# Performance work log

Measured on AMD Instinct MI355X. Metric: run time of the kernel, lower is better.

The kernel has to match this reference:

```python
import jax, jax.numpy as jnp
import numpy as np

D_MODEL = 1024
NUM_HEADS = 16
HEAD_DIM = D_MODEL // NUM_HEADS


def setup_inputs() -> dict:
    key = jax.random.key(0)
    ks = jax.random.split(key, 9)
    B, S = 2, 2048
    s = 1.0 / np.sqrt(D_MODEL)
    inp = {
        "x": jax.random.normal(ks[0], (B, S, D_MODEL), dtype=jnp.float32),
        "Wq": jax.random.normal(ks[1], (D_MODEL, D_MODEL), dtype=jnp.float32) * s,
        "bq": jnp.zeros((D_MODEL,), dtype=jnp.float32),
        "Wk": jax.random.normal(ks[2], (D_MODEL, D_MODEL), dtype=jnp.float32) * s,
        "bk": jnp.zeros((D_MODEL,), dtype=jnp.float32),
        "Wv": jax.random.normal(ks[3], (D_MODEL, D_MODEL), dtype=jnp.float32) * s,
        "bv": jnp.zeros((D_MODEL,), dtype=jnp.float32),
        "Wo": jax.random.normal(ks[4], (D_MODEL, D_MODEL), dtype=jnp.float32) * s,
        "bo": jnpp if False else jnp.zeros((D_MODEL,), dtype=jnp.float32),
    }
    return inp


def reference(x, Wq, bq, Wk, bk, Wv, bv, Wo, bo):
    B, S, D = x.shape
    H, hd = NUM_HEADS, HEAD_DIM
    # QKV projections (Linear: x @ W^T + b), split into heads -> [B,H,S,hd]
    q = (x @ Wq.T + bq).reshape(B, S, H, hd).transpose(0, 2, 1, 3)
    k = (x @ Wk.T + bk).reshape(B, S, H, hd).transpose(0, 2, 1, 3)
    v = (x @ Wv.T + bv).reshape(B, S, H, hd).transpose(0, 2, 1, 3)
    # scores [B,H,S,S]
    scores = jnp.einsum('bhqd,bhkd->bhqk', q, k) / jnp.sqrt(jnp.float32(hd))
    p = jax.nn.softmax(scores, axis=-1)
    out = jnp.einsum('bhqk,bhkd->bhqd', p, v)  # [B,H,S,hd]
    out = out.transpose(0, 2, 1, 3).reshape(B, S, D)
    return out @ Wo.T + bo
```

## Files before the change

### kernel.cpp

```cpp
#include <hip/hip_runtime.h>
#include <hip/hip_bf16.h>
#include <math.h>

typedef __bf16 bf16;
typedef unsigned short u16;
typedef __bf16 bf16x8 __attribute__((ext_vector_type(8)));
typedef __bf16 bf16x4 __attribute__((ext_vector_type(4)));
typedef short  s16x4  __attribute__((ext_vector_type(4)));
typedef float  f32x4  __attribute__((ext_vector_type(4)));

#define D_MODEL 1024
#define NHEAD   16
#define HD      64
#define BATCH   2
#define SEQ     2048
#define MTOT    (BATCH*SEQ)

#define EXPSCALE 0.18033688011116016f

__device__ __forceinline__ void async16(const void* g, void* l) {
    __builtin_amdgcn_global_load_lds(
        (__attribute__((address_space(1))) unsigned int*)g,
        (__attribute__((address_space(3))) unsigned int*)l,
        16, 0, 0);
}

__device__ __forceinline__ f32x4 mfma16(s16x4 a, s16x4 b, f32x4 c) {
    return __builtin_amdgcn_mfma_f32_16x16x16bf16_1k(a, b, c, 0, 0, 0);
}

__global__ __launch_bounds__(256) void cast_kernel(
    const float* __restrict__ x,
    const float* __restrict__ wq, const float* __restrict__ wk,
    const float* __restrict__ wv, const float* __restrict__ wo,
    bf16* __restrict__ xb, bf16* __restrict__ wqb, bf16* __restrict__ wkb,
    bf16* __restrict__ wvb, bf16* __restrict__ wob)
{
    const int z = blockIdx.y;
    const float* src;
    bf16* dst;
    int n;
    if (z == 0)      { src = x;  dst = xb;  n = MTOT * D_MODEL; }
    else if (z == 1) { src = wq; dst = wqb; n = D_MODEL * D_MODEL; }
    else if (z == 2) { src = wk; dst = wkb; n = D_MODEL * D_MODEL; }
    else if (z == 3) { src = wv; dst = wvb; n = D_MODEL * D_MODEL; }
    else             { src = wo; dst = wob; n = D_MODEL * D_MODEL; }

    int i = (blockIdx.x * 256 + threadIdx.x) * 8;
    if (i >= n) return;
    float4 a = *(const float4*)(src + i);
    float4 b = *(const float4*)(src + i + 4);
    bf16x8 o;
    o[0] = (bf16)a.x; o[1] = (bf16)a.y; o[2] = (bf16)a.z; o[3] = (bf16)a.w;
    o[4] = (bf16)b.x; o[5] = (bf16)b.y; o[6] = (bf16)b.z; o[7] = (bf16)b.w;
    *(bf16x8*)(dst + i) = o;
}

__device__ __forceinline__ void gemm_core(const bf16* __restrict__ A,
                                          const bf16* __restrict__ W,
                                          int m0, int n0,
                                          f32x4 acc[4][4],
                                          u16* lA, u16* lB)
{
    const int tid  = threadIdx.x;
    const int lane = tid & 63;
    const int wave = tid >> 6;
    const int wr   = wave >> 1;
    const int wc   = wave & 1;
    const int fr   = lane & 15;
    const int quad = lane >> 4;
    const int sa   = (quad ^ (fr & 3)) * 8;

    #pragma unroll
    for (int mi = 0; mi < 4; ++mi)
        #pragma unroll
        for (int ni = 0; ni < 4; ++ni)
            #pragma unroll
            for (int e = 0; e < 4; ++e)
                acc[mi][ni][e] = 0.0f;

    const int row0 = tid >> 2;
    const int row1 = row0 + 64;
    const int ca   = ((tid & 3) ^ (row0 & 3)) * 8;
    const bf16* gA0 = A + (size_t)(m0 + row0) * 1024 + ca;
    const bf16* gA1 = A + (size_t)(m0 + row1) * 1024 + ca;
    const bf16* gB0 = W + (size_t)(n0 + row0) * 1024 + ca;
    const bf16* gB1 = W + (size_t)(n0 + row1) * 1024 + ca;
    u16* sA0 = lA + (size_t)tid * 8;
    u16* sA1 = lA + (size_t)(tid + 256) * 8;
    u16* sB0 = lB + (size_t)tid * 8;
    u16* sB1 = lB + (size_t)(tid + 256) * 8;

    for (int kt = 0; kt < 1024 / 32; ++kt) {
        __syncthreads();
        async16(gA0 + kt * 32, sA0);
        async16(gA1 + kt * 32, sA1);
        async16(gB0 + kt * 32, sB0);
        async16(gB1 + kt * 32, sB1);
        __syncthreads();

        bf16x8 af[4], bfm[4];
        #pragma unroll
        for (int mi = 0; mi < 4; ++mi)
            af[mi] = *(const bf16x8*)(lA + (wr * 64 + mi * 16 + fr) * 32 + sa);
        #pragma unroll
        for (int ni = 0; ni < 4; ++ni)
            bfm[ni] = *(const bf16x8*)(lB + (wc * 64 + ni * 16 + fr) * 32 + sa);

        #pragma unroll
        for (int mi = 0; mi < 4; ++mi)
            #pragma unroll
            for (int ni = 0; ni < 4; ++ni)
                acc[mi][ni] = __builtin_amdgcn_mfma_f32_16x16x32_bf16(
                    af[mi], bfm[ni], acc[mi][ni], 0, 0, 0);
    }
}

__global__ __launch_bounds__(256) void qkv_kernel(
    const bf16* __restrict__ x,
    const bf16* __restrict__ Wq, const bf16* __restrict__ Wk, const bf16* __restrict__ Wv,
    const float* __restrict__ bq, const float* __restrict__ bk, const float* __restrict__ bv,
    bf16* __restrict__ Q, bf16* __restrict__ K, bf16* __restrict__ Vt)
{
    __shared__ __align__(16) u16 lA[128 * 32];
    __shared__ __align__(16) u16 lB[128 * 32];

    const int z  = blockIdx.z;
    const float* bias = (z == 0) ? bq : (z == 1) ? bk : bv;

    int m0, n0;
    const bf16 *mA, *mB;
    if (z == 2) {
        mA = Wv; mB = x;
        m0 = blockIdx.y * 128;
        n0 = blockIdx.x * 128;
    } else {
        mA = x;  mB = (z == 0) ? Wq : Wk;
        m0 = blockIdx.x * 128;
        n0 = blockIdx.y * 128;
    }

    f32x4 acc[4][4];
    gemm_core(mA, mB, m0, n0, acc, lA, lB);

    const int lane = threadIdx.x & 63;
    const int wave = threadIdx.x >> 6;
    const int wr = wave >> 1, wc = wave & 1;
    const int col = lane & 15, quad = lane >> 4;

    if (z == 2) {
        #pragma unroll
        for (int mi = 0; mi < 4; ++mi) {
            #pragma unroll
            for (int ni = 0; ni < 4; ++ni) {
                #pragma unroll
                for (int r = 0; r < 4; ++r) {
                    int f = m0 + wr * 64 + mi * 16 + quad * 4 + r;
                    int t = n0 + wc * 64 + ni * 16 + col;
                    float v = acc[mi][ni][r] + bias[f];
                    int b = t >> 11, s = t & 2047;
                    int h = f >> 6,  d = f & 63;
                    Vt[((size_t)(b * NHEAD + h) * HD + d) * SEQ + s] = (bf16)v;
                }
            }
        }
    } else {
        const float qs = (z == 0) ? EXPSCALE : 1.0f;
        bf16* o = (z == 0) ? Q : K;
        #pragma unroll
        for (int mi = 0; mi < 4; ++mi) {
            #pragma unroll
            for (int ni = 0; ni < 4; ++ni) {
                #pragma unroll
                for (int r = 0; r < 4; ++r) {
                    int m = m0 + wr * 64 + mi * 16 + quad * 4 + r;
                    int n = n0 + wc * 64 + ni * 16 + col;
                    float v = (acc[mi][ni][r] + bias[n]) * qs;
                    int b = m >> 11, s = m & 2047;
                    int h = n >> 6,  d = n & 63;
                    o[((size_t)(b * NHEAD + h) * SEQ + s) * HD + d] = (bf16)v;
                }
            }
        }
    }
}

__global__ __launch_bounds__(256, 4) void attn_kernel(
    const bf16* __restrict__ Q, const bf16* __restrict__ K,
    const bf16* __restrict__ Vt, bf16* __restrict__ O)
{
    __shared__ __align__(16) u16 lK[64 * 64];
    __shared__ __align__(16) u16 lV[64 * 64];

    const int tid  = threadIdx.x;
    const int lane = tid & 63;
    const int wave = tid >> 6;
    const int col  = lane & 15;
    const int quad = lane >> 4;
    const int bh   = blockIdx.y;
    const int q0   = blockIdx.x * 64;

    const bf16* Qh = Q  + (size_t)bh * SEQ * HD;
    const bf16* Kh = K  + (size_t)bh * SEQ * HD;
    const bf16* Vh = Vt + (size_t)bh * HD * SEQ;

    bf16x8 qf[2];
    #pragma unroll
    for (int ks = 0; ks < 2; ++ks)
        qf[ks] = *(const bf16x8*)(
            Qh + (size_t)(q0 + wave * 16 + col) * HD + ks * 32 + quad * 8);

    f32x4 acc_o[4];
    #pragma unroll
    for (int nd = 0; nd < 4; ++nd)
        #pragma unroll
        for (int e = 0; e < 4; ++e) acc_o[nd][e] = 0.0f;
    float rs = 0.0f;
    const f32x4 zero4 = {0.0f, 0.0f, 0.0f, 0.0f};

    const int r0 = tid >> 3;
    const int r1 = r0 + 32;
    const int g0 = (((tid & 7) ^ (r0 & 7))) * 8;
    const int g1 = (((tid & 7) ^ (r1 & 7))) * 8;
    const bf16* gK0 = Kh + (size_t)r0 * HD + g0;
    const bf16* gK1 = Kh + (size_t)r1 * HD + g1;
    const bf16* gV0 = Vh + (size_t)r0 * SEQ + g0;
    const bf16* gV1 = Vh + (size_t)r1 * SEQ + g1;
    u16* sK0 = lK + (size_t)tid * 8;
    u16* sK1 = lK + (size_t)(tid + 256) * 8;
    u16* sV0 = lV + (size_t)tid * 8;
    u16* sV1 = lV + (size_t)(tid + 256) * 8;

    for (int jt = 0; jt < SEQ / 64; ++jt) {
        __syncthreads();
        async16(gK0 + (size_t)jt * 64 * HD, sK0);
        async16(gK1 + (size_t)jt * 64 * HD, sK1);
        async16(gV0 + jt * 64, sV0);
        async16(gV1 + jt * 64, sV1);
        __syncthreads();

        f32x4 sc[4];
        #pragma unroll
        for (int nj = 0; nj < 4; ++nj) {
            bf16x8 kf0 = *(const bf16x8*)(
                lK + (nj * 16 + col) * 64 + ((0 * 4 + quad) ^ (col & 7)) * 8);
            sc[nj] = __builtin_amdgcn_mfma_f32_16x16x32_bf16(kf0, qf[0], zero4, 0, 0, 0);
        }
        #pragma unroll
        for (int nj = 0; nj < 4; ++nj) {
            bf16x8 kf1 = *(const bf16x8*)(
                lK + (nj * 16 + col) * 64 + ((1 * 4 + quad) ^ (col & 7)) * 8);
            sc[nj] = __builtin_amdgcn_mfma_f32_16x16x32_bf16(kf1, qf[1], sc[nj], 0, 0, 0);
        }

        s16x4 pb[4];
        #pragma unroll
        for (int nj = 0; nj < 4; ++nj) {
            float p0 = __builtin_amdgcn_exp2f(sc[nj][0]);
            float p1 = __builtin_amdgcn_exp2f(sc[nj][1]);
            float p2 = __builtin_amdgcn_exp2f(sc[nj][2]);
            float p3 = __builtin_amdgcn_exp2f(sc[nj][3]);
            rs += (p0 + p1) + (p2 + p3);
            bf16x4 t;
            t[0] = (bf16)p0; t[1] = (bf16)p1; t[2] = (bf16)p2; t[3] = (bf16)p3;
            pb[nj] = __builtin_bit_cast(s16x4, t);
        }

        #pragma unroll
        for (int nj = 0; nj < 4; ++nj) {
            #pragma unroll
            for (int nd = 0; nd < 4; ++nd) {
                int row = nd * 16 + col;
                int jb  = (2 * nj + (quad >> 1)) ^ (row & 7);
                s16x4 vb = *(const s16x4*)(lV + row * 64 + jb * 8 + (quad & 1) * 4);
                acc_o[nd] = mfma16(pb[nj], vb, acc_o[nd]);
            }
        }
    }

    const int b = bh / NHEAD, h = bh % NHEAD;
    float v = rs;
    v += __shfl_xor(v, 16);
    v += __shfl_xor(v, 32);
    float inv = 1.0f / v;
    float invr[4];
    #pragma unroll
    for (int r = 0; r < 4; ++r)
        invr[r] = __shfl(inv, quad * 4 + r);
    #pragma unroll
    for (int nd = 0; nd < 4; ++nd) {
        #pragma unroll
        for (int r = 0; r < 4; ++r) {
            int srow = q0 + wave * 16 + quad * 4 + r;
            int d    = nd * 16 + col;
            float o  = acc_o[nd][r] * invr[r];
            O[((size_t)(b * SEQ + srow)) * D_MODEL + h * HD + d] = (bf16)o;
        }
    }
}

__global__ __launch_bounds__(256) void oproj_kernel(
    const bf16* __restrict__ A, const bf16* __restrict__ Wo,
    const float* __restrict__ bo, float* __restrict__ out)
{
    __shared__ __align__(16) u16 lA[128 * 32];
    __shared__ __align__(16) u16 lB[64 * 32];

    const int m0 = blockIdx.x * 128;
    const int n0 = blockIdx.y * 64;

    const int tid  = threadIdx.x;
    const int lane = tid & 63;
    const int wave = tid >> 6;
    const int wr   = wave >> 1;
    const int wc   = wave & 1;
    const int fr   = lane & 15;
    const int quad = lane >> 4;
    const int sa   = (quad ^ (fr & 3)) * 8;

    f32x4 acc[4][2];
    #pragma unroll
    for (int mi = 0; mi < 4; ++mi)
        #pragma unroll
        for (int ni = 0; ni < 2; ++ni)
            #pragma unroll
            for (int e = 0; e < 4; ++e)
                acc[mi][ni][e] = 0.0f;

    const int row0 = tid >> 2;
    const int row1 = row0 + 64;
    const int ca   = ((tid & 3) ^ (row0 & 3)) * 8;
    const bf16* gA0 = A  + (size_t)(m0 + row0) * 1024 + ca;
    const bf16* gA1 = A  + (size_t)(m0 + row1) * 1024 + ca;
    const bf16* gB0 = Wo + (size_t)(n0 + row0) * 1024 + ca;
    u16* sA0 = lA + (size_t)tid * 8;
    u16* sA1 = lA + (size_t)(tid + 256) * 8;
    u16* sB0 = lB + (size_t)tid * 8;

    for (int kt = 0; kt < 1024 / 32; ++kt) {
        __syncthreads();
        async16(gA0 + kt * 32, sA0);
        async16(gA1 + kt * 32, sA1);
        async16(gB0 + kt * 32, sB0);
        __syncthreads();

        bf16x8 af[4], bfm[2];
        #pragma unroll
        for (int mi = 0; mi < 4; ++mi)
            af[mi] = *(const bf16x8*)(lA + (wr * 64 + mi * 16 + fr) * 32 + sa);
        #pragma unroll
        for (int ni = 0; ni < 2; ++ni)
            bfm[ni] = *(const bf16x8*)(lB + (wc * 32 + ni * 16 + fr) * 32 + sa);

        #pragma unroll
        for (int mi = 0; mi < 4; ++mi)
            #pragma unroll
            for (int ni = 0; ni < 2; ++ni)
                acc[mi][ni] = __builtin_amdgcn_mfma_f32_16x16x32_bf16(
                    af[mi], bfm[ni], acc[mi][ni], 0, 0, 0);
    }

    const int col = fr;
    #pragma unroll
    for (int mi = 0; mi < 4; ++mi) {
        #pragma unroll
        for (int ni = 0; ni < 2; ++ni) {
            #pragma unroll
            for (int r = 0; r < 4; ++r) {
                int m = m0 + wr * 64 + mi * 16 + quad * 4 + r;
                int n = n0 + wc * 32 + ni * 16 + col;
                out[(size_t)m * D_MODEL + n] = acc[mi][ni][r] + bo[n];
            }
        }
    }
}

extern "C" void kernel_launch(void* const* d_in, const int* in_sizes, int n_in,
                              void* d_out, int out_size, void* d_ws, size_t ws_size,
                              hipStream_t stream)
{
    const float* x  = (const float*)d_in[0];
    const float* Wq = (const float*)d_in[1];
    const float* bq = (const float*)d_in[2];
    const float* Wk = (const float*)d_in[3];
    const float* bk = (const float*)d_in[4];
    const float* Wv = (const float*)d_in[5];
    const float* bv = (const float*)d_in[6];
    const float* Wo = (const float*)d_in[7];
    const float* bo = (const float*)d_in[8];
    float* out = (float*)d_out;

    char* ws = (char*)d_ws;
    const size_t XSZ = (size_t)MTOT * D_MODEL * sizeof(bf16);
    const size_t WSZ = (size_t)D_MODEL * D_MODEL * sizeof(bf16);
    bf16* wqb = (bf16*)(ws);
    bf16* wkb = (bf16*)(ws + WSZ);
    bf16* wvb = (bf16*)(ws + 2 * WSZ);
    bf16* wob = (bf16*)(ws + 3 * WSZ);
    bf16* xb  = (bf16*)(ws + 4 * WSZ);
    bf16* Qb  = (bf16*)(ws + 4 * WSZ + XSZ);
    bf16* Kb  = (bf16*)(ws + 4 * WSZ + 2 * XSZ);
    bf16* Vt  = (bf16*)(ws + 4 * WSZ + 3 * XSZ);
    bf16* At  = (bf16*)(ws + 4 * WSZ + 4 * XSZ);

    cast_kernel<<<dim3((MTOT * D_MODEL) / (256 * 8), 5), 256, 0, stream>>>(
        x, Wq, Wk, Wv, Wo, xb, wqb, wkb, wvb, wob);

    qkv_kernel<<<dim3(MTOT / 128, D_MODEL / 128, 3), 256, 0, stream>>>(
        xb, wqb, wkb, wvb, bq, bk, bv, Qb, Kb, Vt);

    attn_kernel<<<dim3(SEQ / 64, BATCH * NHEAD), 256, 0, stream>>>(Qb, Kb, Vt, At);

    oproj_kernel<<<dim3(MTOT / 128, D_MODEL / 64), 256, 0, stream>>>(At, wob, bo, out);
}
```

Before: 202.7 us.

## Split attention KV across waves with LDS reduction; shrink QKV GEMM tile

```diff
diff --git a/kernel.cpp b/kernel.cpp
--- a/kernel.cpp
+++ b/kernel.cpp
@@ -56,11 +56,11 @@
     *(bf16x8*)(dst + i) = o;
 }
 
-__device__ __forceinline__ void gemm_core(const bf16* __restrict__ A,
-                                          const bf16* __restrict__ W,
-                                          int m0, int n0,
-                                          f32x4 acc[4][4],
-                                          u16* lA, u16* lB)
+__device__ __forceinline__ void gemm64_core(const bf16* __restrict__ A,
+                                            const bf16* __restrict__ B,
+                                            int m0, int n0,
+                                            f32x4 acc[4][2],
+                                            u16* lA, u16* lB)
 {
     const int tid  = threadIdx.x;
     const int lane = tid & 63;
@@ -74,7 +74,7 @@
     #pragma unroll
     for (int mi = 0; mi < 4; ++mi)
         #pragma unroll
-        for (int ni = 0; ni < 4; ++ni)
+        for (int ni = 0; ni < 2; ++ni)
             #pragma unroll
             for (int e = 0; e < 4; ++e)
                 acc[mi][ni][e] = 0.0f;
@@ -84,33 +84,30 @@
     const int ca   = ((tid & 3) ^ (row0 & 3)) * 8;
     const bf16* gA0 = A + (size_t)(m0 + row0) * 1024 + ca;
     const bf16* gA1 = A + (size_t)(m0 + row1) * 1024 + ca;
-    const bf16* gB0 = W + (size_t)(n0 + row0) * 1024 + ca;
-    const bf16* gB1 = W + (size_t)(n0 + row1) * 1024 + ca;
+    const bf16* gB0 = B + (size_t)(n0 + row0) * 1024 + ca;
     u16* sA0 = lA + (size_t)tid * 8;
     u16* sA1 = lA + (size_t)(tid + 256) * 8;
     u16* sB0 = lB + (size_t)tid * 8;
-    u16* sB1 = lB + (size_t)(tid + 256) * 8;
 
     for (int kt = 0; kt < 1024 / 32; ++kt) {
         __syncthreads();
         async16(gA0 + kt * 32, sA0);
         async16(gA1 + kt * 32, sA1);
         async16(gB0 + kt * 32, sB0);
-        async16(gB1 + kt * 32, sB1);
         __syncthreads();
 
-        bf16x8 af[4], bfm[4];
+        bf16x8 af[4], bfm[2];
         #pragma unroll
         for (int mi = 0; mi < 4; ++mi)
             af[mi] = *(const bf16x8*)(lA + (wr * 64 + mi * 16 + fr) * 32 + sa);
         #pragma unroll
-        for (int ni = 0; ni < 4; ++ni)
-            bfm[ni] = *(const bf16x8*)(lB + (wc * 64 + ni * 16 + fr) * 32 + sa);
+        for (int ni = 0; ni < 2; ++ni)
+            bfm[ni] = *(const bf16x8*)(lB + (wc * 32 + ni * 16 + fr) * 32 + sa);
 
         #pragma unroll
         for (int mi = 0; mi < 4; ++mi)
             #pragma unroll
-            for (int ni = 0; ni < 4; ++ni)
+            for (int ni = 0; ni < 2; ++ni)
                 acc[mi][ni] = __builtin_amdgcn_mfma_f32_16x16x32_bf16(
                     af[mi], bfm[ni], acc[mi][ni], 0, 0, 0);
     }
@@ -123,25 +120,25 @@
     bf16* __restrict__ Q, bf16* __restrict__ K, bf16* __restrict__ Vt)
 {
     __shared__ __align__(16) u16 lA[128 * 32];
-    __shared__ __align__(16) u16 lB[128 * 32];
-
-    const int z  = blockIdx.z;
-    const float* bias = (z == 0) ? bq : (z == 1) ? bk : bv;
-
+    __shared__ __align__(16) u16 lB[64 * 32];
+
+    const int z = blockIdx.z;
     int m0, n0;
     const bf16 *mA, *mB;
+    const float* bias;
     if (z == 2) {
-        mA = Wv; mB = x;
-        m0 = blockIdx.y * 128;
-        n0 = blockIdx.x * 128;
+        int flat = blockIdx.y * 32 + blockIdx.x;
+        m0 = (flat >> 6) * 128;
+        n0 = (flat & 63) * 64;
+        mA = Wv; mB = x; bias = bv;
     } else {
-        mA = x;  mB = (z == 0) ? Wq : Wk;
         m0 = blockIdx.x * 128;
-        n0 = blockIdx.y * 128;
-    }
-
-    f32x4 acc[4][4];
-    gemm_core(mA, mB, m0, n0, acc, lA, lB);
+        n0 = blockIdx.y * 64;
+        mA = x; mB = (z == 0) ? Wq : Wk; bias = (z == 0) ? bq : bk;
+    }
+
+    f32x4 acc[4][2];
+    gemm64_core(mA, mB, m0, n0, acc, lA, lB);
 
     const int lane = threadIdx.x & 63;
     const int wave = threadIdx.x >> 6;
@@ -152,11 +149,11 @@
         #pragma unroll
         for (int mi = 0; mi < 4; ++mi) {
             #pragma unroll
-            for (int ni = 0; ni < 4; ++ni) {
+            for (int ni = 0; ni < 2; ++ni) {
                 #pragma unroll
                 for (int r = 0; r < 4; ++r) {
                     int f = m0 + wr * 64 + mi * 16 + quad * 4 + r;
-                    int t = n0 + wc * 64 + ni * 16 + col;
+                    int t = n0 + wc * 32 + ni * 16 + col;
                     float v = acc[mi][ni][r] + bias[f];
                     int b = t >> 11, s = t & 2047;
                     int h = f >> 6,  d = f & 63;
@@ -170,11 +167,11 @@
         #pragma unroll
         for (int mi = 0; mi < 4; ++mi) {
             #pragma unroll
-            for (int ni = 0; ni < 4; ++ni) {
+            for (int ni = 0; ni < 2; ++ni) {
                 #pragma unroll
                 for (int r = 0; r < 4; ++r) {
                     int m = m0 + wr * 64 + mi * 16 + quad * 4 + r;
-                    int n = n0 + wc * 64 + ni * 16 + col;
+                    int n = n0 + wc * 32 + ni * 16 + col;
                     float v = (acc[mi][ni][r] + bias[n]) * qs;
                     int b = m >> 11, s = m & 2047;
                     int h = n >> 6,  d = n & 63;
@@ -191,6 +188,8 @@
 {
     __shared__ __align__(16) u16 lK[64 * 64];
     __shared__ __align__(16) u16 lV[64 * 64];
+    __shared__ __align__(16) float lO[64 * 68];
+    __shared__ float lRed[4 * 64];
 
     const int tid  = threadIdx.x;
     const int lane = tid & 63;
@@ -204,19 +203,33 @@
     const bf16* Kh = K  + (size_t)bh * SEQ * HD;
     const bf16* Vh = Vt + (size_t)bh * HD * SEQ;
 
-    bf16x8 qf[2];
-    #pragma unroll
-    for (int ks = 0; ks < 2; ++ks)
-        qf[ks] = *(const bf16x8*)(
-            Qh + (size_t)(q0 + wave * 16 + col) * HD + ks * 32 + quad * 8);
-
-    f32x4 acc_o[4];
-    #pragma unroll
-    for (int nd = 0; nd < 4; ++nd)
-        #pragma unroll
-        for (int e = 0; e < 4; ++e) acc_o[nd][e] = 0.0f;
-    float rs = 0.0f;
+    bf16x8 qf[4][2];
+    #pragma unroll
+    for (int mi = 0; mi < 4; ++mi)
+        #pragma unroll
+        for (int ks = 0; ks < 2; ++ks)
+            qf[mi][ks] = *(const bf16x8*)(
+                Qh + (size_t)(q0 + mi * 16 + col) * HD + ks * 32 + quad * 8);
+
+    f32x4 acc[4][4];
+    #pragma unroll
+    for (int mi = 0; mi < 4; ++mi)
+        #pragma unroll
+        for (int nd = 0; nd < 4; ++nd)
+            #pragma unroll
+            for (int e = 0; e < 4; ++e) acc[mi][nd][e] = 0.0f;
+    float rs[4] = {0.0f, 0.0f, 0.0f, 0.0f};
     const f32x4 zero4 = {0.0f, 0.0f, 0.0f, 0.0f};
+
+    const u16* pkf0 = lK + (wave * 16 + col) * 64 + ((0 + quad) ^ (col & 7)) * 8;
+    const u16* pkf1 = lK + (wave * 16 + col) * 64 + ((4 + quad) ^ (col & 7)) * 8;
+    const u16* pvb[4];
+    #pragma unroll
+    for (int nd = 0; nd < 4; ++nd) {
+        int row = nd * 16 + col;
+        pvb[nd] = lV + row * 64 +
+                  ((2 * wave + (quad >> 1)) ^ (row & 7)) * 8 + (quad & 1) * 4;
+    }
 
     const int r0 = tid >> 3;
     const int r1 = r0 + 32;
@@ -239,64 +252,91 @@
         async16(gV1 + jt * 64, sV1);
         __syncthreads();
 
-        f32x4 sc[4];
-        #pragma unroll
-        for (int nj = 0; nj < 4; ++nj) {
-            bf16x8 kf0 = *(const bf16x8*)(
-                lK + (nj * 16 + col) * 64 + ((0 * 4 + quad) ^ (col & 7)) * 8);
-            sc[nj] = __builtin_amdgcn_mfma_f32_16x16x32_bf16(kf0, qf[0], zero4, 0, 0, 0);
-        }
-        #pragma unroll
-        for (int nj = 0; nj < 4; ++nj) {
-            bf16x8 kf1 = *(const bf16x8*)(
-                lK + (nj * 16 + col) * 64 + ((1 * 4 + quad) ^ (col & 7)) * 8);
-            sc[nj] = __builtin_amdgcn_mfma_f32_16x16x32_bf16(kf1, qf[1], sc[nj], 0, 0, 0);
-        }
+        bf16x8 kf0 = *(const bf16x8*)pkf0;
+        bf16x8 kf1 = *(const bf16x8*)pkf1;
 
         s16x4 pb[4];
         #pragma unroll
-        for (int nj = 0; nj < 4; ++nj) {
-            float p0 = __builtin_amdgcn_exp2f(sc[nj][0]);
-            float p1 = __builtin_amdgcn_exp2f(sc[nj][1]);
-            float p2 = __builtin_amdgcn_exp2f(sc[nj][2]);
-            float p3 = __builtin_amdgcn_exp2f(sc[nj][3]);
-            rs += (p0 + p1) + (p2 + p3);
+        for (int mi = 0; mi < 4; ++mi) {
+            f32x4 sc = __builtin_amdgcn_mfma_f32_16x16x32_bf16(kf0, qf[mi][0], zero4, 0, 0, 0);
+            sc = __builtin_amdgcn_mfma_f32_16x16x32_bf16(kf1, qf[mi][1], sc, 0, 0, 0);
+            float p0 = __builtin_amdgcn_exp2f(sc[0]);
+            float p1 = __builtin_amdgcn_exp2f(sc[1]);
+            float p2 = __builtin_amdgcn_exp2f(sc[2]);
+            float p3 = __builtin_amdgcn_exp2f(sc[3]);
+            rs[mi] += (p0 + p1) + (p2 + p3);
             bf16x4 t;
             t[0] = (bf16)p0; t[1] = (bf16)p1; t[2] = (bf16)p2; t[3] = (bf16)p3;
-            pb[nj] = __builtin_bit_cast(s16x4, t);
-        }
-
-        #pragma unroll
-        for (int nj = 0; nj < 4; ++nj) {
-            #pragma unroll
-            for (int nd = 0; nd < 4; ++nd) {
-                int row = nd * 16 + col;
-                int jb  = (2 * nj + (quad >> 1)) ^ (row & 7);
-                s16x4 vb = *(const s16x4*)(lV + row * 64 + jb * 8 + (quad & 1) * 4);
-                acc_o[nd] = mfma16(pb[nj], vb, acc_o[nd]);
-            }
-        }
-    }
-
-    const int b = bh / NHEAD, h = bh % NHEAD;
-    float v = rs;
-    v += __shfl_xor(v, 16);
-    v += __shfl_xor(v, 32);
-    float inv = 1.0f / v;
-    float invr[4];
-    #pragma unroll
-    for (int r = 0; r < 4; ++r)
-        invr[r] = __shfl(inv, quad * 4 + r);
-    #pragma unroll
-    for (int nd = 0; nd < 4; ++nd) {
-        #pragma unroll
-        for (int r = 0; r < 4; ++r) {
-            int srow = q0 + wave * 16 + quad * 4 + r;
-            int d    = nd * 16 + col;
-            float o  = acc_o[nd][r] * invr[r];
-            O[((size_t)(b * SEQ + srow)) * D_MODEL + h * HD + d] = (bf16)o;
-        }
-    }
+            pb[mi] = __builtin_bit_cast(s16x4, t);
+        }
+
+        #pragma unroll
+        for (int nd = 0; nd < 4; ++nd) {
+            s16x4 vb = *(const s16x4*)pvb[nd];
+            #pragma unroll
+            for (int mi = 0; mi < 4; ++mi)
+                acc[mi][nd] = mfma16(pb[mi], vb, acc[mi][nd]);
+        }
+    }
+
+    #pragma unroll
+    for (int mi = 0; mi < 4; ++mi) {
+        float v = rs[mi];
+        v += __shfl_xor(v, 16);
+        v += __shfl_xor(v, 32);
+        rs[mi] = v;
+    }
+    if (lane < 16) {
+        #pragma unroll
+        for (int mi = 0; mi < 4; ++mi)
+            lRed[wave * 64 + mi * 16 + lane] = rs[mi];
+    }
+
+    if (wave == 0) {
+        #pragma unroll
+        for (int mi = 0; mi < 4; ++mi)
+            #pragma unroll
+            for (int nd = 0; nd < 4; ++nd)
+                #pragma unroll
+                for (int r = 0; r < 4; ++r)
+                    lO[(mi * 16 + quad * 4 + r) * 68 + nd * 16 + col] = acc[mi][nd][r];
+    }
+    __syncthreads();
+    #pragma unroll 1
+    for (int w = 1; w < 4; ++w) {
+        if (wave == w) {
+            #pragma unroll
+            for (int mi = 0; mi < 4; ++mi)
+                #pragma unroll
+                for (int nd = 0; nd < 4; ++nd)
+                    #pragma unroll
+                    for (int r = 0; r < 4; ++r)
+                        lO[(mi * 16 + quad * 4 + r) * 68 + nd * 16 + col] += acc[mi][nd][r];
+        }
+        __syncthreads();
+    }
+
+    const int b = bh >> 4, h = bh & 15;
+    const int row  = wave * 16 + (lane >> 2);
+    const int dblk = (lane & 3) * 16;
+    float lsum = lRed[row] + lRed[64 + row] + lRed[128 + row] + lRed[192 + row];
+    float inv = 1.0f / lsum;
+    const float* src = &lO[row * 68 + dblk];
+    f32x4 v0 = *(const f32x4*)(src);
+    f32x4 v1 = *(const f32x4*)(src + 4);
+    f32x4 v2 = *(const f32x4*)(src + 8);
+    f32x4 v3 = *(const f32x4*)(src + 12);
+    bf16x8 o0, o1;
+    #pragma unroll
+    for (int e = 0; e < 4; ++e) {
+        o0[e]     = (bf16)(v0[e] * inv);
+        o0[e + 4] = (bf16)(v1[e] * inv);
+        o1[e]     = (bf16)(v2[e] * inv);
+        o1[e + 4] = (bf16)(v3[e] * inv);
+    }
+    bf16* dst = O + ((size_t)(b * SEQ + q0 + row)) * D_MODEL + h * HD + dblk;
+    *(bf16x8*)dst = o0;
+    *(bf16x8*)(dst + 8) = o1;
 }
 
 __global__ __launch_bounds__(256) void oproj_kernel(
@@ -309,58 +349,14 @@
     const int m0 = blockIdx.x * 128;
     const int n0 = blockIdx.y * 64;
 
-    const int tid  = threadIdx.x;
-    const int lane = tid & 63;
-    const int wave = tid >> 6;
-    const int wr   = wave >> 1;
-    const int wc   = wave & 1;
-    const int fr   = lane & 15;
-    const int quad = lane >> 4;
-    const int sa   = (quad ^ (fr & 3)) * 8;
-
     f32x4 acc[4][2];
-    #pragma unroll
-    for (int mi = 0; mi < 4; ++mi)
-        #pragma unroll
-        for (int ni = 0; ni < 2; ++ni)
-            #pragma unroll
-            for (int e = 0; e < 4; ++e)
-                acc[mi][ni][e] = 0.0f;
-
-    const int row0 = tid >> 2;
-    const int row1 = row0 + 64;
-    const int ca   = ((tid & 3) ^ (row0 & 3)) * 8;
-    const bf16* gA0 = A  + (size_t)(m0 + row0) * 1024 + ca;
-    const bf16* gA1 = A  + (size_t)(m0 + row1) * 1024 + ca;
-    const bf16* gB0 = Wo + (size_t)(n0 + row0) * 1024 + ca;
-    u16* sA0 = lA + (size_t)tid * 8;
-    u16* sA1 = lA + (size_t)(tid + 256) * 8;
-    u16* sB0 = lB + (size_t)tid * 8;
-
-    for (int kt = 0; kt < 1024 / 32; ++kt) {
-        __syncthreads();
-        async16(gA0 + kt * 32, sA0);
-        async16(gA1 + kt * 32, sA1);
-        async16(gB0 + kt * 32, sB0);
-        __syncthreads();
-
-        bf16x8 af[4], bfm[2];
-        #pragma unroll
-        for (int mi = 0; mi < 4; ++mi)
-            af[mi] = *(const bf16x8*)(lA + (wr * 64 + mi * 16 + fr) * 32 + sa);
-        #pragma unroll
-        for (int ni = 0; ni < 2; ++ni)
-            bfm[ni] = *(const bf16x8*)(lB + (wc * 32 + ni * 16 + fr) * 32 + sa);
-
-        #pragma unroll
-        for (int mi = 0; mi < 4; ++mi)
-            #pragma unroll
-            for (int ni = 0; ni < 2; ++ni)
-                acc[mi][ni] = __builtin_amdgcn_mfma_f32_16x16x32_bf16(
-                    af[mi], bfm[ni], acc[mi][ni], 0, 0, 0);
-    }
-
-    const int col = fr;
+    gemm64_core(A, Wo, m0, n0, acc, lA, lB);
+
+    const int lane = threadIdx.x & 63;
+    const int wave = threadIdx.x >> 6;
+    const int wr = wave >> 1, wc = wave & 1;
+    const int col = lane & 15, quad = lane >> 4;
+
     #pragma unroll
     for (int mi = 0; mi < 4; ++mi) {
         #pragma unroll
@@ -406,7 +402,7 @@
     cast_kernel<<<dim3((MTOT * D_MODEL) / (256 * 8), 5), 256, 0, stream>>>(
         x, Wq, Wk, Wv, Wo, xb, wqb, wkb, wvb, wob);
 
-    qkv_kernel<<<dim3(MTOT / 128, D_MODEL / 128, 3), 256, 0, stream>>>(
+    qkv_kernel<<<dim3(32, 16, 3), 256, 0, stream>>>(
         xb, wqb, wkb, wvb, bq, bk, bv, Qb, Kb, Vt);
 
     attn_kernel<<<dim3(SEQ / 64, BATCH * NHEAD), 256, 0, stream>>>(Qb, Kb, Vt, At);
```

Result: slower. 218.1 us (+7.6%).

## Double K-tile depth in QKV GEMM and KV tile in attention, swap grid order

Applied to the files above, without the earlier changes.

```diff
diff --git a/kernel.cpp b/kernel.cpp
--- a/kernel.cpp
+++ b/kernel.cpp
@@ -69,7 +69,6 @@
     const int wc   = wave & 1;
     const int fr   = lane & 15;
     const int quad = lane >> 4;
-    const int sa   = (quad ^ (fr & 3)) * 8;
 
     #pragma unroll
     for (int mi = 0; mi < 4; ++mi)
@@ -79,40 +78,48 @@
             for (int e = 0; e < 4; ++e)
                 acc[mi][ni][e] = 0.0f;
 
-    const int row0 = tid >> 2;
-    const int row1 = row0 + 64;
-    const int ca   = ((tid & 3) ^ (row0 & 3)) * 8;
-    const bf16* gA0 = A + (size_t)(m0 + row0) * 1024 + ca;
-    const bf16* gA1 = A + (size_t)(m0 + row1) * 1024 + ca;
-    const bf16* gB0 = W + (size_t)(n0 + row0) * 1024 + ca;
-    const bf16* gB1 = W + (size_t)(n0 + row1) * 1024 + ca;
-    u16* sA0 = lA + (size_t)tid * 8;
-    u16* sA1 = lA + (size_t)(tid + 256) * 8;
-    u16* sB0 = lB + (size_t)tid * 8;
-    u16* sB1 = lB + (size_t)(tid + 256) * 8;
-
-    for (int kt = 0; kt < 1024 / 32; ++kt) {
-        __syncthreads();
-        async16(gA0 + kt * 32, sA0);
-        async16(gA1 + kt * 32, sA1);
-        async16(gB0 + kt * 32, sB0);
-        async16(gB1 + kt * 32, sB1);
-        __syncthreads();
-
-        bf16x8 af[4], bfm[4];
-        #pragma unroll
-        for (int mi = 0; mi < 4; ++mi)
-            af[mi] = *(const bf16x8*)(lA + (wr * 64 + mi * 16 + fr) * 32 + sa);
-        #pragma unroll
-        for (int ni = 0; ni < 4; ++ni)
-            bfm[ni] = *(const bf16x8*)(lB + (wc * 64 + ni * 16 + fr) * 32 + sa);
-
-        #pragma unroll
-        for (int mi = 0; mi < 4; ++mi)
+    const int row = tid >> 3;
+    const int ca  = ((tid & 7) ^ (row & 7)) * 8;
+    const bf16* gA[4];
+    const bf16* gB[4];
+    u16 *sA[4], *sB[4];
+    #pragma unroll
+    for (int c = 0; c < 4; ++c) {
+        int slot = tid + c * 256;
+        int r    = row + c * 32;
+        gA[c] = A + (size_t)(m0 + r) * 1024 + ca;
+        gB[c] = W + (size_t)(n0 + r) * 1024 + ca;
+        sA[c] = lA + (size_t)slot * 8;
+        sB[c] = lB + (size_t)slot * 8;
+    }
+
+    for (int kt = 0; kt < 1024 / 64; ++kt) {
+        __syncthreads();
+        #pragma unroll
+        for (int c = 0; c < 4; ++c) {
+            async16(gA[c] + kt * 64, sA[c]);
+            async16(gB[c] + kt * 64, sB[c]);
+        }
+        __syncthreads();
+
+        #pragma unroll
+        for (int ks = 0; ks < 2; ++ks) {
+            const int sa = ((ks * 4 + quad) ^ (fr & 7)) * 8;
+            bf16x8 af[4], bfm[4];
+            #pragma unroll
+            for (int mi = 0; mi < 4; ++mi)
+                af[mi] = *(const bf16x8*)(lA + (wr * 64 + mi * 16 + fr) * 64 + sa);
             #pragma unroll
             for (int ni = 0; ni < 4; ++ni)
-                acc[mi][ni] = __builtin_amdgcn_mfma_f32_16x16x32_bf16(
-                    af[mi], bfm[ni], acc[mi][ni], 0, 0, 0);
+                bfm[ni] = *(const bf16x8*)(lB + (wc * 64 + ni * 16 + fr) * 64 + sa);
+
+            #pragma unroll
+            for (int mi = 0; mi < 4; ++mi)
+                #pragma unroll
+                for (int ni = 0; ni < 4; ++ni)
+                    acc[mi][ni] = __builtin_amdgcn_mfma_f32_16x16x32_bf16(
+                        af[mi], bfm[ni], acc[mi][ni], 0, 0, 0);
+        }
     }
 }
 
@@ -122,20 +129,19 @@
     const float* __restrict__ bq, const float* __restrict__ bk, const float* __restrict__ bv,
     bf16* __restrict__ Q, bf16* __restrict__ K, bf16* __restrict__ Vt)
 {
-    __shared__ __align__(16) u16 lA[128 * 32];
-    __shared__ __align__(16) u16 lB[128 * 32];
-
-    const int z  = blockIdx.z;
-    const float* bias = (z == 0) ? bq : (z == 1) ? bk : bv;
-
+    __shared__ __align__(16) u16 lA[128 * 64];
+    __shared__ __align__(16) u16 lB[128 * 64];
+
+    const int z = blockIdx.z;
     int m0, n0;
     const bf16 *mA, *mB;
+    const float* bias;
     if (z == 2) {
-        mA = Wv; mB = x;
+        mA = Wv; mB = x; bias = bv;
         m0 = blockIdx.y * 128;
         n0 = blockIdx.x * 128;
     } else {
-        mA = x;  mB = (z == 0) ? Wq : Wk;
+        mA = x;  mB = (z == 0) ? Wq : Wk; bias = (z == 0) ? bq : bk;
         m0 = blockIdx.x * 128;
         n0 = blockIdx.y * 128;
     }
@@ -189,16 +195,16 @@
     const bf16* __restrict__ Q, const bf16* __restrict__ K,
     const bf16* __restrict__ Vt, bf16* __restrict__ O)
 {
-    __shared__ __align__(16) u16 lK[64 * 64];
-    __shared__ __align__(16) u16 lV[64 * 64];
+    __shared__ __align__(16) u16 lK[128 * 64];
+    __shared__ __align__(16) u16 lV[64 * 128];
 
     const int tid  = threadIdx.x;
     const int lane = tid & 63;
     const int wave = tid >> 6;
     const int col  = lane & 15;
     const int quad = lane >> 4;
-    const int bh   = blockIdx.y;
-    const int q0   = blockIdx.x * 64;
+    const int bh   = blockIdx.x;
+    const int q0   = blockIdx.y * 64;
 
     const bf16* Qh = Q  + (size_t)bh * SEQ * HD;
     const bf16* Kh = K  + (size_t)bh * SEQ * HD;
@@ -218,48 +224,44 @@
     float rs = 0.0f;
     const f32x4 zero4 = {0.0f, 0.0f, 0.0f, 0.0f};
 
-    const int r0 = tid >> 3;
-    const int r1 = r0 + 32;
-    const int g0 = (((tid & 7) ^ (r0 & 7))) * 8;
-    const int g1 = (((tid & 7) ^ (r1 & 7))) * 8;
-    const bf16* gK0 = Kh + (size_t)r0 * HD + g0;
-    const bf16* gK1 = Kh + (size_t)r1 * HD + g1;
-    const bf16* gV0 = Vh + (size_t)r0 * SEQ + g0;
-    const bf16* gV1 = Vh + (size_t)r1 * SEQ + g1;
-    u16* sK0 = lK + (size_t)tid * 8;
-    u16* sK1 = lK + (size_t)(tid + 256) * 8;
-    u16* sV0 = lV + (size_t)tid * 8;
-    u16* sV1 = lV + (size_t)(tid + 256) * 8;
-
-    for (int jt = 0; jt < SEQ / 64; ++jt) {
-        __syncthreads();
-        async16(gK0 + (size_t)jt * 64 * HD, sK0);
-        async16(gK1 + (size_t)jt * 64 * HD, sK1);
-        async16(gV0 + jt * 64, sV0);
-        async16(gV1 + jt * 64, sV1);
-        __syncthreads();
-
-        f32x4 sc[4];
-        #pragma unroll
-        for (int nj = 0; nj < 4; ++nj) {
-            bf16x8 kf0 = *(const bf16x8*)(
-                lK + (nj * 16 + col) * 64 + ((0 * 4 + quad) ^ (col & 7)) * 8);
-            sc[nj] = __builtin_amdgcn_mfma_f32_16x16x32_bf16(kf0, qf[0], zero4, 0, 0, 0);
-        }
-        #pragma unroll
-        for (int nj = 0; nj < 4; ++nj) {
-            bf16x8 kf1 = *(const bf16x8*)(
-                lK + (nj * 16 + col) * 64 + ((1 * 4 + quad) ^ (col & 7)) * 8);
-            sc[nj] = __builtin_amdgcn_mfma_f32_16x16x32_bf16(kf1, qf[1], sc[nj], 0, 0, 0);
-        }
-
-        s16x4 pb[4];
-        #pragma unroll
-        for (int nj = 0; nj < 4; ++nj) {
-            float p0 = __builtin_amdgcn_exp2f(sc[nj][0]);
-            float p1 = __builtin_amdgcn_exp2f(sc[nj][1]);
-            float p2 = __builtin_amdgcn_exp2f(sc[nj][2]);
-            float p3 = __builtin_amdgcn_exp2f(sc[nj][3]);
+    const int krow = tid >> 3;
+    const int kca  = ((tid & 7) ^ (krow & 7)) * 8;
+    const int vrow = tid >> 4;
+    const int vblk = tid & 15;
+    const int vca  = ((((vblk & 7) ^ (vrow & 7)) | (vblk & 8))) * 8;
+    const bf16* gK[4];
+    const bf16* gV[4];
+    u16 *sK[4], *sV[4];
+    #pragma unroll
+    for (int c = 0; c < 4; ++c) {
+        int slot = tid + c * 256;
+        gK[c] = Kh + (size_t)(krow + c * 32) * HD + kca;
+        gV[c] = Vh + (size_t)(vrow + c * 16) * SEQ + vca;
+        sK[c] = lK + (size_t)slot * 8;
+        sV[c] = lV + (size_t)slot * 8;
+    }
+
+    for (int jt = 0; jt < SEQ / 128; ++jt) {
+        __syncthreads();
+        #pragma unroll
+        for (int c = 0; c < 4; ++c) {
+            async16(gK[c] + (size_t)jt * 128 * HD, sK[c]);
+            async16(gV[c] + jt * 128, sV[c]);
+        }
+        __syncthreads();
+
+        s16x4 pb[8];
+        #pragma unroll
+        for (int nj = 0; nj < 8; ++nj) {
+            const u16* kr = lK + (nj * 16 + col) * 64;
+            bf16x8 kf0 = *(const bf16x8*)(kr + ((0 + quad) ^ (col & 7)) * 8);
+            bf16x8 kf1 = *(const bf16x8*)(kr + ((4 + quad) ^ (col & 7)) * 8);
+            f32x4 sc = __builtin_amdgcn_mfma_f32_16x16x32_bf16(kf0, qf[0], zero4, 0, 0, 0);
+            sc = __builtin_amdgcn_mfma_f32_16x16x32_bf16(kf1, qf[1], sc, 0, 0, 0);
+            float p0 = __builtin_amdgcn_exp2f(sc[0]);
+            float p1 = __builtin_amdgcn_exp2f(sc[1]);
+            float p2 = __builtin_amdgcn_exp2f(sc[2]);
+            float p3 = __builtin_amdgcn_exp2f(sc[3]);
             rs += (p0 + p1) + (p2 + p3);
             bf16x4 t;
             t[0] = (bf16)p0; t[1] = (bf16)p1; t[2] = (bf16)p2; t[3] = (bf16)p3;
@@ -267,18 +269,19 @@
         }
 
         #pragma unroll
-        for (int nj = 0; nj < 4; ++nj) {
+        for (int nj = 0; nj < 8; ++nj) {
             #pragma unroll
             for (int nd = 0; nd < 4; ++nd) {
                 int row = nd * 16 + col;
-                int jb  = (2 * nj + (quad >> 1)) ^ (row & 7);
-                s16x4 vb = *(const s16x4*)(lV + row * 64 + jb * 8 + (quad & 1) * 4);
+                int jb  = 2 * nj + (quad >> 1);
+                int ph  = ((jb & 7) ^ (row & 7)) | (jb & 8);
+                s16x4 vb = *(const s16x4*)(lV + row * 128 + ph * 8 + (quad & 1) * 4);
                 acc_o[nd] = mfma16(pb[nj], vb, acc_o[nd]);
             }
         }
     }
 
-    const int b = bh / NHEAD, h = bh % NHEAD;
+    const int b = bh >> 4, h = bh & 15;
     float v = rs;
     v += __shfl_xor(v, 16);
     v += __shfl_xor(v, 32);
@@ -406,10 +409,10 @@
     cast_kernel<<<dim3((MTOT * D_MODEL) / (256 * 8), 5), 256, 0, stream>>>(
         x, Wq, Wk, Wv, Wo, xb, wqb, wkb, wvb, wob);
 
-    qkv_kernel<<<dim3(MTOT / 128, D_MODEL / 128, 3), 256, 0, stream>>>(
+    qkv_kernel<<<dim3(32, 8, 3), 256, 0, stream>>>(
         xb, wqb, wkb, wvb, bq, bk, bv, Qb, Kb, Vt);
 
-    attn_kernel<<<dim3(SEQ / 64, BATCH * NHEAD), 256, 0, stream>>>(Qb, Kb, Vt, At);
+    attn_kernel<<<dim3(BATCH * NHEAD, SEQ / 64), 256, 0, stream>>>(Qb, Kb, Vt, At);
 
     oproj_kernel<<<dim3(MTOT / 128, D_MODEL / 64), 256, 0, stream>>>(At, wob, bo, out);
 }
```

New measurement: 201.2 us. About the same (-0.7%).
